# Kernel tuning notes

Hardware: AMD Instinct MI355X
Metric: run time of the kernel (lower is better)

Reference implementation:

```python
import jax, jax.numpy as jnp
import numpy as np

DIM = 512; NH = 8; AG = 144; WIN = 18; PS = 12; B = 128; N0 = 320


def _pool_matrix(in_size, out_size):
    # PyTorch AdaptiveAvgPool2d window rule: start=floor(i*in/out), end=ceil((i+1)*in/out)
    P = np.zeros((out_size, in_size), np.float32)
    for i in range(out_size):
        s = (i * in_size) // out_size
        e = -((-(i + 1) * in_size) // out_size)
        P[i, s:e] = 1.0 / (e - s)
    return jnp.asarray(P)


def setup_inputs() -> dict:
    key = jax.random.key(0)
    ks = jax.random.split(key, 12)
    std = 0.02
    return {
        "x": jax.random.normal(ks[0], (B, N0, DIM), jnp.float32),
        "qkv_w": jax.random.normal(ks[1], (DIM, 3 * DIM), jnp.float32) * 0.02,
        "proj_w": jax.random.normal(ks[2], (DIM, DIM), jnp.float32) * 0.02,
        "proj_b": jnp.zeros((DIM,), jnp.float32),
        "dwc_w": jax.random.normal(ks[3], (DIM, 1, 3, 3), jnp.float32) * 0.1,
        "dwc_b": jnp.zeros((DIM,), jnp.float32),
        "an_bias": jax.random.normal(ks[4], (NH, AG, 7, 7), jnp.float32) * std,
        "na_bias": jax.random.normal(ks[5], (NH, AG, 7, 7), jnp.float32) * std,
        "ah_bias": jax.random.normal(ks[6], (1, NH, AG, WIN, 1), jnp.float32) * std,
        "aw_bias": jax.random.normal(ks[7], (1, NH, AG, 1, WIN), jnp.float32) * std,
        "ha_bias": jax.random.normal(ks[8], (1, NH, WIN, 1, AG), jnp.float32) * std,
        "wa_bias": jax.random.normal(ks[9], (1, NH, 1, WIN, AG), jnp.float32) * std,
    }


def reference(x, qkv_w, proj_w, proj_b, dwc_w, dwc_b,
              an_bias, na_bias, ah_bias, aw_bias, ha_bias, wa_bias):
    b, n0, c = x.shape
    x1 = jnp.pad(x, ((0, 0), (2, 2), (0, 0)))          # pad 2 tokens each side
    n = n0 + 4
    h = w = int(n ** 0.5)
    hd = c // NH
    scale = hd ** -0.5

    qkv = x1 @ qkv_w                                    # (b, n, 3c), no bias
    q, k, v = jnp.split(qkv, 3, axis=-1)

    # agent tokens: adaptive avg pool of q on the (h, w) grid to (PS, PS)
    P = _pool_matrix(h, PS)                             # (12, 18)
    qg = q.reshape(b, h, w, c)
    agent = jnp.einsum('oh,bhwc,pw->bopc', P, qg, P).reshape(b, AG, c)

    def heads(t):
        return t.reshape(b, n, NH, hd).transpose(0, 2, 1, 3)
    q, k, v = heads(q), heads(k), heads(v)              # (b, H, n, hd)
    ag = agent.reshape(b, AG, NH, hd).transpose(0, 2, 1, 3)  # (b, H, A, hd)

    # stage 1: agent <- keys  (ac_bias is concatenated then sliced off => no-op)
    pb1 = jax.image.resize(an_bias, (NH, AG, WIN, WIN), 'bilinear').reshape(1, NH, AG, WIN * WIN)
    pb2 = (ah_bias + aw_bias).reshape(1, NH, AG, WIN * WIN)
    agent_attn = jax.nn.softmax(
        jnp.einsum('bhad,bhnd->bhan', ag * scale, k) + pb1 + pb2, axis=-1)
    agent_v = jnp.einsum('bhan,bhnd->bhad', agent_attn, v)   # (b, H, A, hd)

    # stage 2: queries <- agents (ca_bias sliced off => no-op)
    ab1 = jax.image.resize(na_bias, (NH, AG, WIN, WIN), 'bilinear') \
        .reshape(1, NH, AG, WIN * WIN).transpose(0, 1, 3, 2)  # (1, H, n, A)
    ab2 = (ha_bias + wa_bias).reshape(1, NH, WIN * WIN, AG)
    q_attn = jax.nn.softmax(
        jnp.einsum('bhnd,bhad->bhna', q * scale, ag) + ab1 + ab2, axis=-1)
    out = jnp.einsum('bhna,bhad->bhnd', q_attn, agent_v)
    out = out.transpose(0, 2, 1, 3).reshape(b, n, c)

    # depthwise conv skip on v
    vimg = v.transpose(0, 2, 1, 3).reshape(b, h, w, c).transpose(0, 3, 1, 2)  # (b, c, h, w)
    dwc = jax.lax.conv_general_dilated(vimg, dwc_w, (1, 1), 'SAME',
                                       feature_group_count=c)
    dwc = dwc + dwc_b[None, :, None, None]
    out = out + dwc.transpose(0, 2, 3, 1).reshape(b, n, c)

    out = out @ proj_w + proj_b
    return out[:, 2:-2, :]
```

## Files before the change

kernel.cpp:

```cpp
#include <hip/hip_runtime.h>

typedef unsigned short u16;
typedef short bf16x8 __attribute__((ext_vector_type(8)));
typedef float f32x4 __attribute__((ext_vector_type(4)));

#define B_    128
#define N0_   320
#define C_    512
#define NH_   8
#define HD_   64
#define NTOK  324
#define H_    18
#define AG_   144
#define SCALE 0.125f

typedef __attribute__((address_space(3))) unsigned int as3_u32;
typedef __attribute__((address_space(1))) const unsigned int as1_u32;

__device__ __forceinline__ void gl_lds16(const void* g, void* l) {
  __builtin_amdgcn_global_load_lds((as1_u32*)(unsigned long long)g,
                                   (as3_u32*)(unsigned int)(unsigned long long)l,
                                   16, 0, 0);
}

__device__ __forceinline__ float bfu2f(u16 u) {
  union { unsigned int u; float f; } v; v.u = ((unsigned int)u) << 16; return v.f;
}
__device__ __forceinline__ u16 f2bfu(float f) {
  union { float f; unsigned int u; } v; v.f = f;
  unsigned int r = v.u + 0x7fffu + ((v.u >> 16) & 1u);
  return (u16)(r >> 16);
}

__global__ __launch_bounds__(256) void conv_x(const float* __restrict__ x, u16* __restrict__ xp)
{
  const int idx = blockIdx.x * 256 + threadIdx.x;
  const int row = idx >> 6, c8 = idx & 63;
  const int b = row / NTOK, t = row - b * NTOK;
  u16 o[8];
  if (t < 2 || t >= 322) {
    #pragma unroll
    for (int j = 0; j < 8; ++j) o[j] = 0;
  } else {
    const float* src = x + ((size_t)(b * N0_ + (t - 2))) * C_ + c8 * 8;
    const float4 f0 = *(const float4*)(src);
    const float4 f1 = *(const float4*)(src + 4);
    o[0]=f2bfu(f0.x); o[1]=f2bfu(f0.y); o[2]=f2bfu(f0.z); o[3]=f2bfu(f0.w);
    o[4]=f2bfu(f1.x); o[5]=f2bfu(f1.y); o[6]=f2bfu(f1.z); o[7]=f2bfu(f1.w);
  }
  *(bf16x8*)&xp[(size_t)row * C_ + c8 * 8] = *(bf16x8*)o;
}

__global__ __launch_bounds__(256) void tconv(const float* __restrict__ W, u16* __restrict__ Wt, int ncols)
{
  __shared__ float T[64][65];
  const int k0 = blockIdx.x * 64, n0 = blockIdx.y * 64;
  const int tid = threadIdx.x;
  const int rr = tid >> 4, cc = tid & 15;
  #pragma unroll
  for (int i = 0; i < 4; ++i) {
    const float4 f = *(const float4*)&W[(size_t)(k0 + i * 16 + rr) * ncols + n0 + cc * 4];
    T[i * 16 + rr][cc * 4 + 0] = f.x; T[i * 16 + rr][cc * 4 + 1] = f.y;
    T[i * 16 + rr][cc * 4 + 2] = f.z; T[i * 16 + rr][cc * 4 + 3] = f.w;
  }
  __syncthreads();
  #pragma unroll
  for (int i = 0; i < 4; ++i) {
    const int n = i * 16 + rr;
    ushort4 u;
    u.x = f2bfu(T[cc * 4 + 0][n]); u.y = f2bfu(T[cc * 4 + 1][n]);
    u.z = f2bfu(T[cc * 4 + 2][n]); u.w = f2bfu(T[cc * 4 + 3][n]);
    *(ushort4*)&Wt[(size_t)(n0 + n) * 512 + k0 + cc * 4] = u;
  }
}

template<int MODE>
__global__ __launch_bounds__(256) void mfma_gemm(
    const u16* __restrict__ A, const u16* __restrict__ Bt,
    u16* __restrict__ qb, u16* __restrict__ kb, u16* __restrict__ vb,
    const float* __restrict__ bias, float* __restrict__ outf)
{
  __shared__ __align__(16) u16 As[128 * 64];
  __shared__ __align__(16) u16 Bs[128 * 64];
  const int bx = blockIdx.x;
  const int by = blockIdx.y;
  const int tid = threadIdx.x;
  const int wv = tid >> 6, lane = tid & 63;
  const int lr = lane & 15, lk = lane >> 4;
  const int wr = wv >> 1, wc = wv & 1;
  const int si = lane >> 3, slot = lane & 7;

  size_t arow_src[4];
  #pragma unroll
  for (int jj = 0; jj < 4; ++jj) {
    const int rl = (wv * 4 + jj) * 8 + si;
    const int r = by * 128 + rl;
    if (MODE == 0) {
      arow_src[jj] = (size_t)r * 512;
    } else {
      const int b2 = r / N0_, ii = r - b2 * N0_;
      arow_src[jj] = ((size_t)b2 * 8 * NTOK + (ii + 2)) * 64;
    }
  }

  f32x4 acc[4][4] = {};
  for (int k0 = 0; k0 < 512; k0 += 64) {
    __syncthreads();
    #pragma unroll
    for (int jj = 0; jj < 4; ++jj) {
      const int rl = (wv * 4 + jj) * 8 + si;
      const int c = slot ^ (rl & 7);
      const u16* asrc = (MODE == 0)
          ? (A + arow_src[jj] + k0 + c * 8)
          : (A + arow_src[jj] + (size_t)(k0 >> 6) * (NTOK * 64) + c * 8);
      gl_lds16(asrc, (char*)As + (wv * 4 + jj) * 1024);
      gl_lds16(Bt + (size_t)(bx * 128 + rl) * 512 + k0 + c * 8,
               (char*)Bs + (wv * 4 + jj) * 1024);
    }
    __syncthreads();
    #pragma unroll
    for (int kk = 0; kk < 2; ++kk) {
      bf16x8 af[4], bf[4];
      #pragma unroll
      for (int m = 0; m < 4; ++m) {
        const int row = wr * 64 + m * 16 + lr;
        af[m] = *(const bf16x8*)((const char*)As + row * 128 + (((kk * 4 + lk) ^ (row & 7)) << 4));
      }
      #pragma unroll
      for (int n = 0; n < 4; ++n) {
        const int row = wc * 64 + n * 16 + lr;
        bf[n] = *(const bf16x8*)((const char*)Bs + row * 128 + (((kk * 4 + lk) ^ (row & 7)) << 4));
      }
      #pragma unroll
      for (int m = 0; m < 4; ++m)
        #pragma unroll
        for (int n = 0; n < 4; ++n)
          acc[m][n] = __builtin_amdgcn_mfma_f32_16x16x32_bf16(af[m], bf[n], acc[m][n], 0, 0, 0);
    }
  }

  if (MODE == 0) {
    const int mat = (bx * 128) >> 9;
    u16* outp = (mat == 0) ? qb : (mat == 1) ? kb : vb;
    #pragma unroll
    for (int m = 0; m < 4; ++m) {
      #pragma unroll
      for (int r = 0; r < 4; ++r) {
        const int row = by * 128 + wr * 64 + m * 16 + lk * 4 + r;
        const int b = row / NTOK, t = row - b * NTOK;
        #pragma unroll
        for (int n = 0; n < 4; ++n) {
          const int col = bx * 128 + wc * 64 + n * 16 + lr;
          const int rem = col & 511, h = rem >> 6, d = rem & 63;
          outp[(((size_t)(b * NH_ + h)) * NTOK + t) * HD_ + d] = f2bfu(acc[m][n][r]);
        }
      }
    }
  } else {
    #pragma unroll
    for (int m = 0; m < 4; ++m) {
      #pragma unroll
      for (int r = 0; r < 4; ++r) {
        const int row = by * 128 + wr * 64 + m * 16 + lk * 4 + r;
        #pragma unroll
        for (int n = 0; n < 4; ++n) {
          const int col = bx * 128 + wc * 64 + n * 16 + lr;
          outf[(size_t)row * C_ + col] = acc[m][n][r] + bias[col];
        }
      }
    }
  }
}

__global__ void bias_kernel(const float* __restrict__ an, const float* __restrict__ na,
                            const float* __restrict__ ah, const float* __restrict__ aw,
                            const float* __restrict__ ha, const float* __restrict__ wa,
                            u16* __restrict__ bAN, u16* __restrict__ bNA)
{
  const int blk = blockIdx.x;
  const int h = blk / AG_, a = blk - h * AG_;
  const int tid = threadIdx.x;
  if (tid >= NTOK) return;
  const int y = tid / H_, x = tid - y * H_;
  float cy = (y + 0.5f) * (7.0f / 18.0f) - 0.5f; cy = fminf(fmaxf(cy, 0.f), 6.f);
  float cx = (x + 0.5f) * (7.0f / 18.0f) - 0.5f; cx = fminf(fmaxf(cx, 0.f), 6.f);
  const int y0 = (int)floorf(cy); const float ty = cy - y0; const int y1 = min(y0 + 1, 6);
  const int x0 = (int)floorf(cx); const float tx = cx - x0; const int x1 = min(x0 + 1, 6);
  const float w00 = (1.f - ty) * (1.f - tx), w01 = (1.f - ty) * tx;
  const float w10 = ty * (1.f - tx), w11 = ty * tx;
  const float* anp = an + (size_t)blk * 49;
  const float* nap = na + (size_t)blk * 49;
  const float van = w00 * anp[y0*7+x0] + w01 * anp[y0*7+x1] + w10 * anp[y1*7+x0] + w11 * anp[y1*7+x1];
  const float vna = w00 * nap[y0*7+x0] + w01 * nap[y0*7+x1] + w10 * nap[y1*7+x0] + w11 * nap[y1*7+x1];
  bAN[(size_t)blk * NTOK + tid] = f2bfu(van + ah[(size_t)blk * H_ + y] + aw[(size_t)blk * H_ + x]);
  bNA[((size_t)h * NTOK + tid) * AG_ + a] =
      f2bfu(vna + ha[((size_t)h * H_ + y) * AG_ + a] + wa[((size_t)h * H_ + x) * AG_ + a]);
}

__global__ __launch_bounds__(512) void pool_kernel(const u16* __restrict__ qb, u16* __restrict__ agb)
{
  const int blk = blockIdx.x;
  const int b = blk / AG_, a = blk - b * AG_;
  const int o = a / 12, pc = a - o * 12;
  const int y0 = (3 * o) >> 1, x0 = (3 * pc) >> 1;
  const int c = threadIdx.x; const int h = c >> 6, d = c & 63;
  const size_t base = ((size_t)(b * NH_ + h)) * NTOK * HD_ + d;
  const int t00 = (y0 * H_ + x0) * HD_;
  const float v = bfu2f(qb[base + t00]) + bfu2f(qb[base + t00 + HD_])
                + bfu2f(qb[base + t00 + H_ * HD_]) + bfu2f(qb[base + t00 + H_ * HD_ + HD_]);
  agb[((size_t)(b * NH_ + h)) * AG_ * HD_ + a * HD_ + d] = f2bfu(0.25f * v);
}

__global__ __launch_bounds__(576) void fused_attn(
    const u16* __restrict__ kb, const u16* __restrict__ vb,
    const u16* __restrict__ qb, const u16* __restrict__ agb,
    const u16* __restrict__ bAN, const u16* __restrict__ bNA,
    const float* __restrict__ dwc_w, const float* __restrict__ dwc_b,
    u16* __restrict__ aob)
{
  __shared__ __align__(16) u16 vT[64 * 360];
  __shared__ __align__(16) u16 avT[64 * 168];
  __shared__ __align__(16) u16 pW[9][16][40];
  __shared__ u16 wL[64 * 10];
  const int bh = blockIdx.x, h = bh & 7;
  const int tid = threadIdx.x;
  const int mt = tid >> 6;
  const int l = tid & 63, lr = l & 15, lk = l >> 4;

  for (int idx = tid; idx < 640; idx += 576) {
    const int d = idx / 10, j = idx - d * 10;
    wL[idx] = f2bfu((j < 9) ? dwc_w[(size_t)(h * 64 + d) * 9 + j] : dwc_b[h * 64 + d]);
  }
  for (int idx = tid; idx < 128; idx += 576)
    *(bf16x8*)&avT[(idx >> 1) * 168 + 144 + (idx & 1) * 8] = (bf16x8){0,0,0,0,0,0,0,0};

  const u16* vsrc = vb + (size_t)bh * NTOK * HD_;
  for (int idx = tid; idx < 64 * 45; idx += 576) {
    const int d = idx & 63, c = idx >> 6;
    bf16x8 tv;
    #pragma unroll
    for (int j = 0; j < 8; ++j) {
      const int n = c * 8 + j;
      tv[j] = (n < NTOK) ? (short)vsrc[(size_t)n * HD_ + d] : (short)0;
    }
    *(bf16x8*)&vT[d * 360 + c * 8] = tv;
  }

  const u16* aga = agb + ((size_t)bh * AG_ + mt * 16 + lr) * HD_ + lk * 8;
  const bf16x8 a0 = *(const bf16x8*)(aga);
  const bf16x8 a1 = *(const bf16x8*)(aga + 32);

  f32x4 acc[21];
  const u16* kbase = kb + (size_t)bh * NTOK * HD_ + lk * 8;
  __builtin_amdgcn_s_setprio(1);
  #pragma unroll
  for (int nt = 0; nt < 21; ++nt) {
    const bf16x8 b0 = *(const bf16x8*)(kbase + (size_t)(nt * 16 + lr) * HD_);
    const bf16x8 b1 = *(const bf16x8*)(kbase + (size_t)(nt * 16 + lr) * HD_ + 32);
    f32x4 c = {0.f, 0.f, 0.f, 0.f};
    c = __builtin_amdgcn_mfma_f32_16x16x32_bf16(a0, b0, c, 0, 0, 0);
    c = __builtin_amdgcn_mfma_f32_16x16x32_bf16(a1, b1, c, 0, 0, 0);
    acc[nt] = c;
  }
  __builtin_amdgcn_s_setprio(0);

  const u16* bb = bAN + ((size_t)h * AG_ + mt * 16) * NTOK;
  float mx[4] = {-1e30f, -1e30f, -1e30f, -1e30f};
  #pragma unroll
  for (int nt = 0; nt < 21; ++nt) {
    const int col = nt * 16 + lr;
    const bool valid = (nt < 20) || (lr < 4);
    #pragma unroll
    for (int r = 0; r < 4; ++r) {
      float s = -1e30f;
      if (valid) s = acc[nt][r] * SCALE + bfu2f(bb[(lk * 4 + r) * NTOK + col]);
      acc[nt][r] = s;
      mx[r] = fmaxf(mx[r], s);
    }
  }
  #pragma unroll
  for (int r = 0; r < 4; ++r) {
    #pragma unroll
    for (int o = 1; o < 16; o <<= 1) mx[r] = fmaxf(mx[r], __shfl_xor(mx[r], o));
  }
  float sm[4] = {0.f, 0.f, 0.f, 0.f};
  #pragma unroll
  for (int nt = 0; nt < 21; ++nt) {
    #pragma unroll
    for (int r = 0; r < 4; ++r) {
      const float e = __expf(acc[nt][r] - mx[r]);
      acc[nt][r] = e;
      sm[r] += e;
    }
  }
  #pragma unroll
  for (int r = 0; r < 4; ++r) {
    #pragma unroll
    for (int o = 1; o < 16; o <<= 1) sm[r] += __shfl_xor(sm[r], o);
    sm[r] = 1.0f / sm[r];
  }

  __syncthreads();

  f32x4 ov[4];
  #pragma unroll
  for (int nt2 = 0; nt2 < 4; ++nt2) ov[nt2] = (f32x4){0.f, 0.f, 0.f, 0.f};
  for (int ks = 0; ks < 11; ++ks) {
    #pragma unroll
    for (int half = 0; half < 2; ++half) {
      const int nt = 2 * ks + half;
      #pragma unroll
      for (int r = 0; r < 4; ++r)
        pW[mt][lk * 4 + r][half * 16 + lr] = (nt < 21) ? f2bfu(acc[nt][r] * sm[r]) : (u16)0;
    }
    const bf16x8 pa = *(const bf16x8*)&pW[mt][lr][lk * 8];
    __builtin_amdgcn_s_setprio(1);
    #pragma unroll
    for (int nt2 = 0; nt2 < 4; ++nt2) {
      const bf16x8 vf = *(const bf16x8*)&vT[(nt2 * 16 + lr) * 360 + ks * 32 + lk * 8];
      ov[nt2] = __builtin_amdgcn_mfma_f32_16x16x32_bf16(pa, vf, ov[nt2], 0, 0, 0);
    }
    __builtin_amdgcn_s_setprio(0);
  }
  #pragma unroll
  for (int nt2 = 0; nt2 < 4; ++nt2) {
    ushort4 u;
    u.x = f2bfu(ov[nt2][0]); u.y = f2bfu(ov[nt2][1]);
    u.z = f2bfu(ov[nt2][2]); u.w = f2bfu(ov[nt2][3]);
    *(ushort4*)&avT[(nt2 * 16 + lr) * 168 + mt * 16 + lk * 4] = u;
  }

  __syncthreads();

  u16* aout = aob + (size_t)bh * NTOK * HD_;
  for (int mt2 = mt; mt2 < 21; mt2 += 9) {
    const int arow = min(mt2 * 16 + lr, NTOK - 1);
    const u16* qa = qb + ((size_t)bh * NTOK + arow) * HD_ + lk * 8;
    const bf16x8 qa0 = *(const bf16x8*)(qa);
    const bf16x8 qa1 = *(const bf16x8*)(qa + 32);

    f32x4 acc2[9];
    __builtin_amdgcn_s_setprio(1);
    #pragma unroll
    for (int nt = 0; nt < 9; ++nt) {
      const u16* bp = agb + ((size_t)bh * AG_ + nt * 16 + lr) * HD_ + lk * 8;
      f32x4 c = {0.f, 0.f, 0.f, 0.f};
      c = __builtin_amdgcn_mfma_f32_16x16x32_bf16(qa0, *(const bf16x8*)(bp), c, 0, 0, 0);
      c = __builtin_amdgcn_mfma_f32_16x16x32_bf16(qa1, *(const bf16x8*)(bp + 32), c, 0, 0, 0);
      acc2[nt] = c;
    }
    __builtin_amdgcn_s_setprio(0);

    float mx2[4] = {-1e30f, -1e30f, -1e30f, -1e30f};
    #pragma unroll
    for (int nt = 0; nt < 9; ++nt) {
      #pragma unroll
      for (int r = 0; r < 4; ++r) {
        const int trow = min(mt2 * 16 + lk * 4 + r, NTOK - 1);
        const float s = acc2[nt][r] * SCALE + bfu2f(bNA[((size_t)h * NTOK + trow) * AG_ + nt * 16 + lr]);
        acc2[nt][r] = s;
        mx2[r] = fmaxf(mx2[r], s);
      }
    }
    #pragma unroll
    for (int r = 0; r < 4; ++r) {
      #pragma unroll
      for (int o = 1; o < 16; o <<= 1) mx2[r] = fmaxf(mx2[r], __shfl_xor(mx2[r], o));
    }
    float sm2[4] = {0.f, 0.f, 0.f, 0.f};
    #pragma unroll
    for (int nt = 0; nt < 9; ++nt) {
      #pragma unroll
      for (int r = 0; r < 4; ++r) {
        const float e = __expf(acc2[nt][r] - mx2[r]);
        acc2[nt][r] = e;
        sm2[r] += e;
      }
    }
    #pragma unroll
    for (int r = 0; r < 4; ++r) {
      #pragma unroll
      for (int o = 1; o < 16; o <<= 1) sm2[r] += __shfl_xor(sm2[r], o);
      sm2[r] = 1.0f / sm2[r];
    }

    f32x4 ov2[4];
    #pragma unroll
    for (int dt = 0; dt < 4; ++dt) ov2[dt] = (f32x4){0.f, 0.f, 0.f, 0.f};
    for (int ks = 0; ks < 5; ++ks) {
      #pragma unroll
      for (int half = 0; half < 2; ++half) {
        const int nt = 2 * ks + half;
        #pragma unroll
        for (int r = 0; r < 4; ++r)
          pW[mt][lk * 4 + r][half * 16 + lr] = (nt < 9) ? f2bfu(acc2[nt][r] * sm2[r]) : (u16)0;
      }
      const bf16x8 pa = *(const bf16x8*)&pW[mt][lr][lk * 8];
      __builtin_amdgcn_s_setprio(1);
      #pragma unroll
      for (int dt = 0; dt < 4; ++dt) {
        const bf16x8 vf = *(const bf16x8*)&avT[(dt * 16 + lr) * 168 + ks * 32 + lk * 8];
        ov2[dt] = __builtin_amdgcn_mfma_f32_16x16x32_bf16(vf, pa, ov2[dt], 0, 0, 0);
      }
      __builtin_amdgcn_s_setprio(0);
    }

    const int t = mt2 * 16 + lr;
    if (t < NTOK) {
      const int y = t / H_, x = t - y * H_;
      #pragma unroll
      for (int dt = 0; dt < 4; ++dt) {
        ushort4 u;
        #pragma unroll
        for (int r = 0; r < 4; ++r) {
          const int d = dt * 16 + lk * 4 + r;
          float conv = bfu2f(wL[d * 10 + 9]);
          #pragma unroll
          for (int ky = 0; ky < 3; ++ky) {
            const int yy = y + ky - 1;
            if (yy < 0 || yy >= H_) continue;
            #pragma unroll
            for (int kx = 0; kx < 3; ++kx) {
              const int xc = x + kx - 1;
              if (xc < 0 || xc >= H_) continue;
              conv += bfu2f(wL[d * 10 + ky * 3 + kx]) * bfu2f(vT[d * 360 + yy * H_ + xc]);
            }
          }
          ((u16*)&u)[r] = f2bfu(ov2[dt][r] + conv);
        }
        *(ushort4*)&aout[(size_t)t * HD_ + dt * 16 + lk * 4] = u;
      }
    }
  }
}

extern "C" void kernel_launch(void* const* d_in, const int* in_sizes, int n_in,
                              void* d_out, int out_size, void* d_ws, size_t ws_size,
                              hipStream_t stream)
{
  (void)in_sizes; (void)n_in; (void)out_size;
  const float* x      = (const float*)d_in[0];
  const float* qkv_w  = (const float*)d_in[1];
  const float* proj_w = (const float*)d_in[2];
  const float* proj_b = (const float*)d_in[3];
  const float* dwc_w  = (const float*)d_in[4];
  const float* dwc_b  = (const float*)d_in[5];
  const float* an     = (const float*)d_in[6];
  const float* na     = (const float*)d_in[7];
  const float* ah     = (const float*)d_in[8];
  const float* aw     = (const float*)d_in[9];
  const float* ha     = (const float*)d_in[10];
  const float* wa     = (const float*)d_in[11];

  char* ws = (char*)d_ws;
  const size_t QB  = (size_t)B_ * NH_ * NTOK * HD_ * 2;
  const size_t AGB = (size_t)B_ * NH_ * AG_  * HD_ * 2;
  const size_t BB  = (size_t)NH_ * AG_ * NTOK * 2;
  const size_t WQ  = (size_t)1536 * 512 * 2;
  const size_t WP  = (size_t)512 * 512 * 2;
  u16* qb    = (u16*)(ws);
  u16* kb    = (u16*)(ws + QB);
  u16* vb    = (u16*)(ws + 2 * QB);
  u16* xp    = (u16*)(ws + 3 * QB);
  u16* agb   = (u16*)(ws + 3 * QB);
  u16* bAN   = (u16*)(ws + 3 * QB + AGB);
  u16* bNA   = (u16*)(ws + 3 * QB + AGB + BB);
  u16* wqkvT = (u16*)(ws + 4 * QB);
  u16* wprojT= (u16*)(ws + 4 * QB + WQ);
  u16* aob   = kb;
  if (ws_size < 4 * QB + WQ + WP) return;

  conv_x   <<<dim3(B_ * NTOK * 64 / 256), dim3(256), 0, stream>>>(x, xp);
  tconv    <<<dim3(8, 24), dim3(256), 0, stream>>>(qkv_w, wqkvT, 1536);
  tconv    <<<dim3(8, 8),  dim3(256), 0, stream>>>(proj_w, wprojT, 512);
  mfma_gemm<0><<<dim3(12, 324), dim3(256), 0, stream>>>(xp, wqkvT, qb, kb, vb, nullptr, nullptr);
  pool_kernel<<<dim3(B_ * AG_),  dim3(512), 0, stream>>>(qb, agb);
  bias_kernel<<<dim3(NH_ * AG_), dim3(324), 0, stream>>>(an, na, ah, aw, ha, wa, bAN, bNA);
  fused_attn<<<dim3(B_ * NH_), dim3(576), 0, stream>>>(kb, vb, qb, agb, bAN, bNA, dwc_w, dwc_b, aob);
  mfma_gemm<1><<<dim3(4, 320), dim3(256), 0, stream>>>(aob, wprojT, nullptr, nullptr, nullptr, proj_b, (float*)d_out);
}
```

Measured before the change: 502.0 us.

## Split fused agent attention into stage1, depthwise-conv, and stage2 kernels

Splits the single fused attention kernel into three kernels. Stage 1 computes agent_v and writes it transposed to global memory. A separate depthwise-conv kernel writes the conv result into the output buffer. Stage 2 computes query attention and accumulates into that buffer. The bias tables are stored transposed so each lane can read its bias values as one vectorised ushort4, and the block order is changed to head-major. The split aims to cut LDS use and register pressure for better occupancy, at the cost of extra global round trips and more kernel launches.

```diff
diff --git a/kernel.cpp b/kernel.cpp
--- a/kernel.cpp
+++ b/kernel.cpp
@@ -175,7 +175,7 @@
 __global__ void bias_kernel(const float* __restrict__ an, const float* __restrict__ na,
                             const float* __restrict__ ah, const float* __restrict__ aw,
                             const float* __restrict__ ha, const float* __restrict__ wa,
-                            u16* __restrict__ bAN, u16* __restrict__ bNA)
+                            u16* __restrict__ bANT, u16* __restrict__ bNAT)
 {
   const int blk = blockIdx.x;
   const int h = blk / AG_, a = blk - h * AG_;
@@ -192,8 +192,9 @@
   const float* nap = na + (size_t)blk * 49;
   const float van = w00 * anp[y0*7+x0] + w01 * anp[y0*7+x1] + w10 * anp[y1*7+x0] + w11 * anp[y1*7+x1];
   const float vna = w00 * nap[y0*7+x0] + w01 * nap[y0*7+x1] + w10 * nap[y1*7+x0] + w11 * nap[y1*7+x1];
-  bAN[(size_t)blk * NTOK + tid] = f2bfu(van + ah[(size_t)blk * H_ + y] + aw[(size_t)blk * H_ + x]);
-  bNA[((size_t)h * NTOK + tid) * AG_ + a] =
+  bANT[((size_t)h * NTOK + tid) * AG_ + a] =
+      f2bfu(van + ah[(size_t)blk * H_ + y] + aw[(size_t)blk * H_ + x]);
+  bNAT[((size_t)h * AG_ + a) * NTOK + tid] =
       f2bfu(vna + ha[((size_t)h * H_ + y) * AG_ + a] + wa[((size_t)h * H_ + x) * AG_ + a]);
 }
 
@@ -211,28 +212,53 @@
   agb[((size_t)(b * NH_ + h)) * AG_ * HD_ + a * HD_ + d] = f2bfu(0.25f * v);
 }
 
-__global__ __launch_bounds__(576) void fused_attn(
+__global__ __launch_bounds__(512) void dwc_kernel(
+    const u16* __restrict__ vb, const float* __restrict__ dwc_w,
+    const float* __restrict__ dwc_b, u16* __restrict__ aob)
+{
+  __shared__ __align__(16) u16 vL[NTOK * 64];
+  const int hb = blockIdx.x, h = hb >> 7, b = hb & 127;
+  const int bh = b * NH_ + h;
+  const int tid = threadIdx.x;
+  const bf16x8* vs = (const bf16x8*)(vb + (size_t)bh * NTOK * HD_);
+  for (int idx = tid; idx < NTOK * 8; idx += 512)
+    ((bf16x8*)vL)[idx] = vs[idx];
+  const int d = tid & 63, tg = tid >> 6;
+  float w9[9];
+  #pragma unroll
+  for (int j = 0; j < 9; ++j) w9[j] = dwc_w[(size_t)(h * 64 + d) * 9 + j];
+  const float cb = dwc_b[h * 64 + d];
+  __syncthreads();
+  u16* aout = aob + (size_t)bh * NTOK * HD_;
+  for (int t = tg; t < NTOK; t += 8) {
+    const int y = t / H_, x = t - y * H_;
+    float conv = cb;
+    #pragma unroll
+    for (int ky = 0; ky < 3; ++ky) {
+      const int yy = y + ky - 1;
+      if (yy < 0 || yy >= H_) continue;
+      #pragma unroll
+      for (int kx = 0; kx < 3; ++kx) {
+        const int xc = x + kx - 1;
+        if (xc < 0 || xc >= H_) continue;
+        conv += w9[ky * 3 + kx] * bfu2f(vL[(yy * H_ + xc) * 64 + d]);
+      }
+    }
+    aout[(size_t)t * HD_ + d] = f2bfu(conv);
+  }
+}
+
+__global__ __launch_bounds__(576) void stage1_k(
     const u16* __restrict__ kb, const u16* __restrict__ vb,
-    const u16* __restrict__ qb, const u16* __restrict__ agb,
-    const u16* __restrict__ bAN, const u16* __restrict__ bNA,
-    const float* __restrict__ dwc_w, const float* __restrict__ dwc_b,
-    u16* __restrict__ aob)
+    const u16* __restrict__ agb, const u16* __restrict__ bANT,
+    u16* __restrict__ avbT)
 {
   __shared__ __align__(16) u16 vT[64 * 360];
-  __shared__ __align__(16) u16 avT[64 * 168];
   __shared__ __align__(16) u16 pW[9][16][40];
-  __shared__ u16 wL[64 * 10];
-  const int bh = blockIdx.x, h = bh & 7;
+  const int hb = blockIdx.x, h = hb >> 7, b = hb & 127;
+  const int bh = b * NH_ + h;
   const int tid = threadIdx.x;
-  const int mt = tid >> 6;
-  const int l = tid & 63, lr = l & 15, lk = l >> 4;
-
-  for (int idx = tid; idx < 640; idx += 576) {
-    const int d = idx / 10, j = idx - d * 10;
-    wL[idx] = f2bfu((j < 9) ? dwc_w[(size_t)(h * 64 + d) * 9 + j] : dwc_b[h * 64 + d]);
-  }
-  for (int idx = tid; idx < 128; idx += 576)
-    *(bf16x8*)&avT[(idx >> 1) * 168 + 144 + (idx & 1) * 8] = (bf16x8){0,0,0,0,0,0,0,0};
+  const int mt = tid >> 6, l = tid & 63, lr = l & 15, lk = l >> 4;
 
   const u16* vsrc = vb + (size_t)bh * NTOK * HD_;
   for (int idx = tid; idx < 64 * 45; idx += 576) {
@@ -264,16 +290,18 @@
   }
   __builtin_amdgcn_s_setprio(0);
 
-  const u16* bb = bAN + ((size_t)h * AG_ + mt * 16) * NTOK;
   float mx[4] = {-1e30f, -1e30f, -1e30f, -1e30f};
   #pragma unroll
   for (int nt = 0; nt < 21; ++nt) {
-    const int col = nt * 16 + lr;
+    const int t = nt * 16 + lr;
     const bool valid = (nt < 20) || (lr < 4);
+    ushort4 b4 = make_ushort4(0, 0, 0, 0);
+    if (valid)
+      b4 = *(const ushort4*)&bANT[((size_t)h * NTOK + t) * AG_ + mt * 16 + lk * 4];
     #pragma unroll
     for (int r = 0; r < 4; ++r) {
       float s = -1e30f;
-      if (valid) s = acc[nt][r] * SCALE + bfu2f(bb[(lk * 4 + r) * NTOK + col]);
+      if (valid) s = acc[nt][r] * SCALE + bfu2f(((const u16*)&b4)[r]);
       acc[nt][r] = s;
       mx[r] = fmaxf(mx[r], s);
     }
@@ -322,18 +350,50 @@
     }
     __builtin_amdgcn_s_setprio(0);
   }
+
+  __syncthreads();
+
+  u16* avTL = vT;
   #pragma unroll
   for (int nt2 = 0; nt2 < 4; ++nt2) {
     ushort4 u;
     u.x = f2bfu(ov[nt2][0]); u.y = f2bfu(ov[nt2][1]);
     u.z = f2bfu(ov[nt2][2]); u.w = f2bfu(ov[nt2][3]);
-    *(ushort4*)&avT[(nt2 * 16 + lr) * 168 + mt * 16 + lk * 4] = u;
-  }
+    *(ushort4*)&avTL[(nt2 * 16 + lr) * 168 + mt * 16 + lk * 4] = u;
+  }
+  for (int idx = tid; idx < 128; idx += 576)
+    *(bf16x8*)&avTL[(idx >> 1) * 168 + 144 + (idx & 1) * 8] = (bf16x8){0,0,0,0,0,0,0,0};
 
   __syncthreads();
 
+  u16* dst = avbT + (size_t)bh * 64 * 160;
+  for (int idx = tid; idx < 64 * 20; idx += 576) {
+    const int d = idx / 20, c = idx - d * 20;
+    *(bf16x8*)&dst[d * 160 + c * 8] = *(const bf16x8*)&avTL[d * 168 + c * 8];
+  }
+}
+
+__global__ __launch_bounds__(512, 6) void stage2_k(
+    const u16* __restrict__ qb, const u16* __restrict__ agb,
+    const u16* __restrict__ avbT, const u16* __restrict__ bNAT,
+    u16* __restrict__ aob)
+{
+  __shared__ __align__(16) u16 avT[64 * 168];
+  __shared__ __align__(16) u16 pW[8][16][40];
+  const int hb = blockIdx.x, h = hb >> 7, b = hb & 127;
+  const int bh = b * NH_ + h;
+  const int tid = threadIdx.x;
+  const int wv = tid >> 6, l = tid & 63, lr = l & 15, lk = l >> 4;
+
+  const u16* src = avbT + (size_t)bh * 64 * 160;
+  for (int idx = tid; idx < 64 * 20; idx += 512) {
+    const int d = idx / 20, c = idx - d * 20;
+    *(bf16x8*)&avT[d * 168 + c * 8] = *(const bf16x8*)&src[d * 160 + c * 8];
+  }
+  __syncthreads();
+
   u16* aout = aob + (size_t)bh * NTOK * HD_;
-  for (int mt2 = mt; mt2 < 21; mt2 += 9) {
+  for (int mt2 = wv; mt2 < 21; mt2 += 8) {
     const int arow = min(mt2 * 16 + lr, NTOK - 1);
     const u16* qa = qb + ((size_t)bh * NTOK + arow) * HD_ + lk * 8;
     const bf16x8 qa0 = *(const bf16x8*)(qa);
@@ -352,12 +412,13 @@
     __builtin_amdgcn_s_setprio(0);
 
     float mx2[4] = {-1e30f, -1e30f, -1e30f, -1e30f};
+    const int t0 = mt2 * 16 + lk * 4;
     #pragma unroll
     for (int nt = 0; nt < 9; ++nt) {
+      const ushort4 b4 = *(const ushort4*)&bNAT[((size_t)h * AG_ + nt * 16 + lr) * NTOK + t0];
       #pragma unroll
       for (int r = 0; r < 4; ++r) {
-        const int trow = min(mt2 * 16 + lk * 4 + r, NTOK - 1);
-        const float s = acc2[nt][r] * SCALE + bfu2f(bNA[((size_t)h * NTOK + trow) * AG_ + nt * 16 + lr]);
+        const float s = acc2[nt][r] * SCALE + bfu2f(((const u16*)&b4)[r]);
         acc2[nt][r] = s;
         mx2[r] = fmaxf(mx2[r], s);
       }
@@ -393,9 +454,9 @@
         const int nt = 2 * ks + half;
         #pragma unroll
         for (int r = 0; r < 4; ++r)
-          pW[mt][lk * 4 + r][half * 16 + lr] = (nt < 9) ? f2bfu(acc2[nt][r] * sm2[r]) : (u16)0;
-      }
-      const bf16x8 pa = *(const bf16x8*)&pW[mt][lr][lk * 8];
+          pW[wv][lk * 4 + r][half * 16 + lr] = (nt < 9) ? f2bfu(acc2[nt][r] * sm2[r]) : (u16)0;
+      }
+      const bf16x8 pa = *(const bf16x8*)&pW[wv][lr][lk * 8];
       __builtin_amdgcn_s_setprio(1);
       #pragma unroll
       for (int dt = 0; dt < 4; ++dt) {
@@ -407,28 +468,15 @@
 
     const int t = mt2 * 16 + lr;
     if (t < NTOK) {
-      const int y = t / H_, x = t - y * H_;
       #pragma unroll
       for (int dt = 0; dt < 4; ++dt) {
-        ushort4 u;
-        #pragma unroll
-        for (int r = 0; r < 4; ++r) {
-          const int d = dt * 16 + lk * 4 + r;
-          float conv = bfu2f(wL[d * 10 + 9]);
-          #pragma unroll
-          for (int ky = 0; ky < 3; ++ky) {
-            const int yy = y + ky - 1;
-            if (yy < 0 || yy >= H_) continue;
-            #pragma unroll
-            for (int kx = 0; kx < 3; ++kx) {
-              const int xc = x + kx - 1;
-              if (xc < 0 || xc >= H_) continue;
-              conv += bfu2f(wL[d * 10 + ky * 3 + kx]) * bfu2f(vT[d * 360 + yy * H_ + xc]);
-            }
-          }
-          ((u16*)&u)[r] = f2bfu(ov2[dt][r] + conv);
-        }
-        *(ushort4*)&aout[(size_t)t * HD_ + dt * 16 + lk * 4] = u;
+        u16* p = &aout[(size_t)t * HD_ + dt * 16 + lk * 4];
+        ushort4 u = *(ushort4*)p;
+        u.x = f2bfu(bfu2f(u.x) + ov2[dt][0]);
+        u.y = f2bfu(bfu2f(u.y) + ov2[dt][1]);
+        u.z = f2bfu(bfu2f(u.z) + ov2[dt][2]);
+        u.w = f2bfu(bfu2f(u.w) + ov2[dt][3]);
+        *(ushort4*)p = u;
       }
     }
   }
@@ -453,29 +501,33 @@
   const float* wa     = (const float*)d_in[11];
 
   char* ws = (char*)d_ws;
-  const size_t QB  = (size_t)B_ * NH_ * NTOK * HD_ * 2;
-  const size_t AGB = (size_t)B_ * NH_ * AG_  * HD_ * 2;
-  const size_t BB  = (size_t)NH_ * AG_ * NTOK * 2;
-  const size_t WQ  = (size_t)1536 * 512 * 2;
-  const size_t WP  = (size_t)512 * 512 * 2;
+  const size_t QB   = (size_t)B_ * NH_ * NTOK * HD_ * 2;
+  const size_t AGB  = (size_t)B_ * NH_ * AG_  * HD_ * 2;
+  const size_t AVTB = (size_t)B_ * NH_ * 64 * 160 * 2;
+  const size_t BB   = (size_t)NH_ * AG_ * NTOK * 2 + 64;
+  const size_t WQ   = (size_t)1536 * 512 * 2;
+  const size_t WP   = (size_t)512 * 512 * 2;
   u16* qb    = (u16*)(ws);
   u16* kb    = (u16*)(ws + QB);
   u16* vb    = (u16*)(ws + 2 * QB);
   u16* xp    = (u16*)(ws + 3 * QB);
   u16* agb   = (u16*)(ws + 3 * QB);
-  u16* bAN   = (u16*)(ws + 3 * QB + AGB);
-  u16* bNA   = (u16*)(ws + 3 * QB + AGB + BB);
+  u16* avbT  = (u16*)(ws + 3 * QB + AGB);
+  u16* bANT  = (u16*)(ws + 3 * QB + AGB + AVTB);
   u16* wqkvT = (u16*)(ws + 4 * QB);
   u16* wprojT= (u16*)(ws + 4 * QB + WQ);
+  u16* bNAT  = (u16*)(ws + 4 * QB + WQ + WP);
   u16* aob   = kb;
-  if (ws_size < 4 * QB + WQ + WP) return;
+  if (ws_size < 4 * QB + WQ + WP + BB) return;
 
   conv_x   <<<dim3(B_ * NTOK * 64 / 256), dim3(256), 0, stream>>>(x, xp);
   tconv    <<<dim3(8, 24), dim3(256), 0, stream>>>(qkv_w, wqkvT, 1536);
   tconv    <<<dim3(8, 8),  dim3(256), 0, stream>>>(proj_w, wprojT, 512);
   mfma_gemm<0><<<dim3(12, 324), dim3(256), 0, stream>>>(xp, wqkvT, qb, kb, vb, nullptr, nullptr);
   pool_kernel<<<dim3(B_ * AG_),  dim3(512), 0, stream>>>(qb, agb);
-  bias_kernel<<<dim3(NH_ * AG_), dim3(324), 0, stream>>>(an, na, ah, aw, ha, wa, bAN, bNA);
-  fused_attn<<<dim3(B_ * NH_), dim3(576), 0, stream>>>(kb, vb, qb, agb, bAN, bNA, dwc_w, dwc_b, aob);
+  bias_kernel<<<dim3(NH_ * AG_), dim3(324), 0, stream>>>(an, na, ah, aw, ha, wa, bANT, bNAT);
+  stage1_k <<<dim3(NH_ * B_), dim3(576), 0, stream>>>(kb, vb, agb, bANT, avbT);
+  dwc_kernel<<<dim3(NH_ * B_), dim3(512), 0, stream>>>(vb, dwc_w, dwc_b, aob);
+  stage2_k <<<dim3(NH_ * B_), dim3(512), 0, stream>>>(qb, agb, avbT, bNAT, aob);
   mfma_gemm<1><<<dim3(4, 320), dim3(256), 0, stream>>>(aob, wprojT, nullptr, nullptr, nullptr, proj_b, (float*)d_out);
 }
```

New measurement: 497.7 us. About the same (-0.9%).
